# Performance work log

Measured on AMD Instinct MI355X. Metric: run time of the kernel, lower is better.

## Reference

```python
import jax, jax.numpy as jnp
import numpy as np

N = 8192
IN_F = 256
OUT_F = 128

def setup_inputs() -> dict:
    key = jax.random.key(0)
    k1, k2, k3, k4, k5 = jax.random.split(key, 5)
    adjacency_matrix = jax.random.uniform(k1, (N, N), dtype=jnp.float32)
    node_features = jax.random.normal(k2, (N, IN_F), dtype=jnp.float32)
    # nn.Linear(in_features, out_features): W is [out, in], b is [out]
    W = jax.random.normal(k3, (OUT_F, IN_F), dtype=jnp.float32) / np.sqrt(IN_F)
    b = jax.random.normal(k4, (OUT_F,), dtype=jnp.float32) * 0.01
    attn_weights = jax.random.normal(k5, (OUT_F, OUT_F), dtype=jnp.float32)
    return {"adjacency_matrix": adjacency_matrix, "node_features": node_features,
            "W": W, "b": b, "attn_weights": attn_weights}

def reference(adjacency_matrix, node_features, W, b, attn_weights):
    # h = Linear(node_features): [N, out]
    h = node_features @ W.T + b
    # bilinear scores: h @ (A @ h^T) -> [N, N]
    scores = jnp.einsum('nd,de,me->nm', h, attn_weights, h)
    attn = jax.nn.softmax(scores, axis=1)
    # weighted aggregation: [N, N] @ [N, out]
    h_agg = attn @ h
    return h_agg
```

## Files before the change

kernel.cpp:

```cpp
#include <hip/hip_runtime.h>
#include <hip/hip_bf16.h>
#include <stdint.h>


#define NN 8192
#define INF_ 256
#define D 128
#define BQ 64
#define BK 64
#define KSPLIT 4
#define KSEG (NN / KSPLIT)
#define L2E 1.44269504088896340736f

typedef __attribute__((ext_vector_type(8))) short bf16x8;
typedef __attribute__((ext_vector_type(4))) float f32x4;
typedef __attribute__((ext_vector_type(4))) unsigned int uint4v;

__global__ __launch_bounds__(256) void prep_kernel(
    const float* __restrict__ X, const float* __restrict__ W,
    const float* __restrict__ bias, const float* __restrict__ A,
    __hip_bfloat16* __restrict__ h_hi, __hip_bfloat16* __restrict__ h_lo,
    __hip_bfloat16* __restrict__ q_hi, __hip_bfloat16* __restrict__ q_lo,
    __hip_bfloat16* __restrict__ ht)
{
    __shared__ float xs[32][INF_];
    __shared__ float hs[32][D];
    const int tid  = threadIdx.x;
    const int row0 = blockIdx.x * 32;

    {
        const f32x4* Xv = (const f32x4*)(X + (size_t)row0 * INF_);
        f32x4* xsv = (f32x4*)&xs[0][0];
        #pragma unroll
        for (int i = 0; i < 8; ++i) xsv[tid + i*256] = Xv[tid + i*256];
    }
    __syncthreads();

    const int c  = tid & 127;
    const int rh = tid >> 7;

    float acc[16];
    #pragma unroll
    for (int r = 0; r < 16; ++r) acc[r] = 0.f;
    const f32x4* Wv = (const f32x4*)(W + (size_t)c * INF_);
    for (int k4 = 0; k4 < INF_/4; ++k4) {
        f32x4 w4 = Wv[k4];
        #pragma unroll
        for (int r = 0; r < 16; ++r) {
            f32x4 x4 = ((const f32x4*)&xs[rh*16 + r][0])[k4];
            acc[r] += x4[0]*w4[0] + x4[1]*w4[1] + x4[2]*w4[2] + x4[3]*w4[3];
        }
    }
    const float bc = bias[c];
    #pragma unroll
    for (int r = 0; r < 16; ++r) {
        const int row = rh*16 + r;
        const float hv = acc[r] + bc;
        hs[row][c] = hv;
        const __hip_bfloat16 hi = __float2bfloat16(hv);
        const float lo = hv - __bfloat162float(hi);
        h_hi[(size_t)(row0+row)*D + c] = hi;
        h_lo[(size_t)(row0+row)*D + c] = __float2bfloat16(lo);
        ht  [(size_t)c*NN + row0 + row] = hi;
    }
    __syncthreads();

    float acc2[16];
    #pragma unroll
    for (int r = 0; r < 16; ++r) acc2[r] = 0.f;
    for (int d4 = 0; d4 < D/4; ++d4) {
        f32x4 hv4[16];
        #pragma unroll
        for (int r = 0; r < 16; ++r) hv4[r] = ((const f32x4*)&hs[rh*16 + r][0])[d4];
        #pragma unroll
        for (int dd = 0; dd < 4; ++dd) {
            const float a = A[(size_t)(d4*4 + dd)*D + c];
            #pragma unroll
            for (int r = 0; r < 16; ++r) acc2[r] += hv4[r][dd] * a;
        }
    }
    #pragma unroll
    for (int r = 0; r < 16; ++r) {
        const int row = rh*16 + r;
        const float tv = acc2[r];
        const __hip_bfloat16 hi = __float2bfloat16(tv);
        const float lo = tv - __bfloat162float(hi);
        q_hi[(size_t)(row0+row)*D + c] = hi;
        q_lo[(size_t)(row0+row)*D + c] = __float2bfloat16(lo);
    }
}

__global__ __launch_bounds__(256) void flash_kernel(
    const __hip_bfloat16* __restrict__ q_hi, const __hip_bfloat16* __restrict__ q_lo,
    const __hip_bfloat16* __restrict__ k_hi, const __hip_bfloat16* __restrict__ k_lo,
    const __hip_bfloat16* __restrict__ ht,
    float* __restrict__ opart, float* __restrict__ mpart, float* __restrict__ lpart)
{
    __shared__ __hip_bfloat16 khi[BK][136];
    __shared__ __hip_bfloat16 klo[BK][136];
    __shared__ __hip_bfloat16 vt[D][72];
    __shared__ __hip_bfloat16 pbuf[4][16][72];

    const int tid  = threadIdx.x;
    const int wave = tid >> 6;
    const int lane = tid & 63;
    const int l16  = lane & 15;
    const int quad = lane >> 4;
    const int q0    = blockIdx.x * BQ;
    const int split = blockIdx.y;
    const int jbase = split * KSEG;

    bf16x8 aqh[4], aql[4];
    {
        const size_t qrow = (size_t)q0 + wave*16 + l16;
        const __hip_bfloat16* qhp = q_hi + qrow*D;
        const __hip_bfloat16* qlp = q_lo + qrow*D;
        #pragma unroll
        for (int t = 0; t < 4; ++t) {
            aqh[t] = *(const bf16x8*)(qhp + t*32 + quad*8);
            aql[t] = *(const bf16x8*)(qlp + t*32 + quad*8);
        }
    }

    f32x4 oacc[8];
    #pragma unroll
    for (int i = 0; i < 8; ++i) oacc[i] = (f32x4){0.f, 0.f, 0.f, 0.f};
    float mi[4], li[4];
    #pragma unroll
    for (int r = 0; r < 4; ++r) { mi[r] = -1e30f; li[r] = 0.f; }

    for (int it = 0; it < KSEG/BK; ++it) {
        const int j0 = jbase + it * BK;
        __syncthreads();
        #pragma unroll
        for (int i = 0; i < 4; ++i) {
            const int chunk = tid + i*256;
            const int r  = chunk >> 4, c8 = chunk & 15;
            *(uint4v*)(&khi[r][c8*8]) = *(const uint4v*)(k_hi + (size_t)(j0+r)*D + c8*8);
            *(uint4v*)(&klo[r][c8*8]) = *(const uint4v*)(k_lo + (size_t)(j0+r)*D + c8*8);
            const int dd = chunk >> 3, cc = chunk & 7;
            *(uint4v*)(&vt[dd][cc*8]) = *(const uint4v*)(ht + (size_t)dd*NN + j0 + cc*8);
        }
        __syncthreads();

        f32x4 s[4];
        #pragma unroll
        for (int jt = 0; jt < 4; ++jt) {
            f32x4 acc = (f32x4){0.f, 0.f, 0.f, 0.f};
            #pragma unroll
            for (int t = 0; t < 4; ++t) {
                const bf16x8 bh = *(const bf16x8*)(&khi[jt*16 + l16][t*32 + quad*8]);
                const bf16x8 bl = *(const bf16x8*)(&klo[jt*16 + l16][t*32 + quad*8]);
                acc = __builtin_amdgcn_mfma_f32_16x16x32_bf16(aql[t], bh, acc, 0, 0, 0);
                acc = __builtin_amdgcn_mfma_f32_16x16x32_bf16(aqh[t], bl, acc, 0, 0, 0);
                acc = __builtin_amdgcn_mfma_f32_16x16x32_bf16(aqh[t], bh, acc, 0, 0, 0);
            }
            s[jt] = acc;
        }

        float p[4][4];
        #pragma unroll
        for (int r = 0; r < 4; ++r) {
            float v = fmaxf(fmaxf(s[0][r], s[1][r]), fmaxf(s[2][r], s[3][r]));
            #pragma unroll
            for (int m = 1; m < 16; m <<= 1) v = fmaxf(v, __shfl_xor(v, m, 64));
            const float mnew  = fmaxf(mi[r], v);
            const float alpha = exp2f((mi[r] - mnew) * L2E);
            mi[r] = mnew;
            #pragma unroll
            for (int dt = 0; dt < 8; ++dt) oacc[dt][r] *= alpha;
            float sum = 0.f;
            #pragma unroll
            for (int jt = 0; jt < 4; ++jt) {
                const float pv = exp2f((s[jt][r] - mnew) * L2E);
                p[jt][r] = pv;
                sum += pv;
            }
            #pragma unroll
            for (int m = 1; m < 16; m <<= 1) sum += __shfl_xor(sum, m, 64);
            li[r] = li[r] * alpha + sum;
        }

        #pragma unroll
        for (int r = 0; r < 4; ++r)
            #pragma unroll
            for (int jt = 0; jt < 4; ++jt)
                pbuf[wave][quad*4 + r][jt*16 + l16] = __float2bfloat16(p[jt][r]);
        __syncthreads();

        bf16x8 ap[2];
        #pragma unroll
        for (int u = 0; u < 2; ++u)
            ap[u] = *(const bf16x8*)(&pbuf[wave][l16][u*32 + quad*8]);
        #pragma unroll
        for (int dt = 0; dt < 8; ++dt)
            #pragma unroll
            for (int u = 0; u < 2; ++u) {
                const bf16x8 bv = *(const bf16x8*)(&vt[dt*16 + l16][u*32 + quad*8]);
                oacc[dt] = __builtin_amdgcn_mfma_f32_16x16x32_bf16(ap[u], bv, oacc[dt], 0, 0, 0);
            }
    }

    const int qrow_base = q0 + wave*16;
    float* op = opart + ((size_t)split * NN + qrow_base) * D;
    #pragma unroll
    for (int r = 0; r < 4; ++r) {
        const int m = quad*4 + r;
        #pragma unroll
        for (int dt = 0; dt < 8; ++dt)
            op[(size_t)m*D + dt*16 + l16] = oacc[dt][r];
    }
    if (l16 == 0) {
        #pragma unroll
        for (int r = 0; r < 4; ++r) {
            mpart[(size_t)split*NN + qrow_base + quad*4 + r] = mi[r];
            lpart[(size_t)split*NN + qrow_base + quad*4 + r] = li[r];
        }
    }
}

__global__ __launch_bounds__(256) void combine_kernel(
    const float* __restrict__ opart, const float* __restrict__ mpart,
    const float* __restrict__ lpart, float* __restrict__ out)
{
    const int idx = blockIdx.x * 256 + threadIdx.x;
    const int q = idx >> 7;
    float m = -1e30f;
    #pragma unroll
    for (int s = 0; s < KSPLIT; ++s) m = fmaxf(m, mpart[(size_t)s*NN + q]);
    float z = 0.f, o = 0.f;
    #pragma unroll
    for (int s = 0; s < KSPLIT; ++s) {
        const float w = exp2f((mpart[(size_t)s*NN + q] - m) * L2E);
        z += lpart[(size_t)s*NN + q] * w;
        o += opart[(size_t)s*NN*D + idx] * w;
    }
    out[idx] = o / z;
}

extern "C" void kernel_launch(void* const* d_in, const int* in_sizes, int n_in,
                              void* d_out, int out_size, void* d_ws, size_t ws_size,
                              hipStream_t stream)
{
    const float* X = (const float*)d_in[1];
    const float* W = (const float*)d_in[2];
    const float* b = (const float*)d_in[3];
    const float* A = (const float*)d_in[4];
    float* out = (float*)d_out;

    char* ws = (char*)d_ws;
    __hip_bfloat16* h_hi = (__hip_bfloat16*)(ws);
    __hip_bfloat16* h_lo = (__hip_bfloat16*)(ws + (size_t)(2u  << 20));
    __hip_bfloat16* q_hi = (__hip_bfloat16*)(ws + (size_t)(4u  << 20));
    __hip_bfloat16* q_lo = (__hip_bfloat16*)(ws + (size_t)(6u  << 20));
    __hip_bfloat16* ht   = (__hip_bfloat16*)(ws + (size_t)(8u  << 20));
    float* opart = (float*)(ws + (size_t)(10u << 20));
    float* mpart = (float*)(ws + (size_t)(26u << 20));
    float* lpart = (float*)(ws + (size_t)(26u << 20) + (256u << 10));

    prep_kernel<<<NN/32, 256, 0, stream>>>(X, W, b, A, h_hi, h_lo, q_hi, q_lo, ht);
    flash_kernel<<<dim3(NN/BQ, KSPLIT), 256, 0, stream>>>(
        q_hi, q_lo, h_hi, h_lo, ht, opart, mpart, lpart);
    combine_kernel<<<(NN*D)/256, 256, 0, stream>>>(opart, mpart, lpart, out);
}
```

Before: 481.7 us.

## Compute transposed scores so softmax P stays in registers, double query rows per wave

The flash kernel now computes S^T with K as the MFMA A operand, so each lane holds a full column of probabilities. That lets P feed the PV MFMA straight from registers, removing the LDS pbuf round trip and the extra barrier. Each wave now handles 32 query rows (BQ=128), which reuses every loaded K/V fragment twice, and KSPLIT goes from 4 to 8 to keep the grid size the same. The costs are higher register pressure (launch bounds set to 2 blocks), more partial output traffic into a larger combine step, and V fragments built from two 8-byte LDS reads.

```diff
diff --git a/kernel.cpp b/kernel.cpp
--- a/kernel.cpp
+++ b/kernel.cpp
@@ -6,13 +6,14 @@
 #define NN 8192
 #define INF_ 256
 #define D 128
-#define BQ 64
+#define BQ 128
 #define BK 64
-#define KSPLIT 4
+#define KSPLIT 8
 #define KSEG (NN / KSPLIT)
 #define L2E 1.44269504088896340736f
 
 typedef __attribute__((ext_vector_type(8))) short bf16x8;
+typedef __attribute__((ext_vector_type(4))) short bf16x4;
 typedef __attribute__((ext_vector_type(4))) float f32x4;
 typedef __attribute__((ext_vector_type(4))) unsigned int uint4v;
 
@@ -90,7 +91,7 @@
     }
 }
 
-__global__ __launch_bounds__(256) void flash_kernel(
+__global__ __launch_bounds__(256, 2) void flash_kernel(
     const __hip_bfloat16* __restrict__ q_hi, const __hip_bfloat16* __restrict__ q_lo,
     const __hip_bfloat16* __restrict__ k_hi, const __hip_bfloat16* __restrict__ k_lo,
     const __hip_bfloat16* __restrict__ ht,
@@ -99,7 +100,6 @@
     __shared__ __hip_bfloat16 khi[BK][136];
     __shared__ __hip_bfloat16 klo[BK][136];
     __shared__ __hip_bfloat16 vt[D][72];
-    __shared__ __hip_bfloat16 pbuf[4][16][72];
 
     const int tid  = threadIdx.x;
     const int wave = tid >> 6;
@@ -110,27 +110,28 @@
     const int split = blockIdx.y;
     const int jbase = split * KSEG;
 
-    bf16x8 aqh[4], aql[4];
-    {
-        const size_t qrow = (size_t)q0 + wave*16 + l16;
+    bf16x8 bqh[2][4], bql[2][4];
+    #pragma unroll
+    for (int it = 0; it < 2; ++it) {
+        const size_t qrow = (size_t)q0 + wave*32 + it*16 + l16;
         const __hip_bfloat16* qhp = q_hi + qrow*D;
         const __hip_bfloat16* qlp = q_lo + qrow*D;
         #pragma unroll
         for (int t = 0; t < 4; ++t) {
-            aqh[t] = *(const bf16x8*)(qhp + t*32 + quad*8);
-            aql[t] = *(const bf16x8*)(qlp + t*32 + quad*8);
-        }
-    }
-
-    f32x4 oacc[8];
-    #pragma unroll
-    for (int i = 0; i < 8; ++i) oacc[i] = (f32x4){0.f, 0.f, 0.f, 0.f};
-    float mi[4], li[4];
-    #pragma unroll
-    for (int r = 0; r < 4; ++r) { mi[r] = -1e30f; li[r] = 0.f; }
-
-    for (int it = 0; it < KSEG/BK; ++it) {
-        const int j0 = jbase + it * BK;
+            bqh[it][t] = *(const bf16x8*)(qhp + t*32 + quad*8);
+            bql[it][t] = *(const bf16x8*)(qlp + t*32 + quad*8);
+        }
+    }
+
+    f32x4 oacc[2][8];
+    #pragma unroll
+    for (int it = 0; it < 2; ++it)
+        #pragma unroll
+        for (int i = 0; i < 8; ++i) oacc[it][i] = (f32x4){0.f, 0.f, 0.f, 0.f};
+    float mi[2] = {-1e30f, -1e30f}, li[2] = {0.f, 0.f};
+
+    for (int tile = 0; tile < KSEG/BK; ++tile) {
+        const int j0 = jbase + tile * BK;
         __syncthreads();
         #pragma unroll
         for (int i = 0; i < 4; ++i) {
@@ -143,78 +144,99 @@
         }
         __syncthreads();
 
-        f32x4 s[4];
+        f32x4 st[2][4];
         #pragma unroll
         for (int jt = 0; jt < 4; ++jt) {
-            f32x4 acc = (f32x4){0.f, 0.f, 0.f, 0.f};
             #pragma unroll
             for (int t = 0; t < 4; ++t) {
-                const bf16x8 bh = *(const bf16x8*)(&khi[jt*16 + l16][t*32 + quad*8]);
-                const bf16x8 bl = *(const bf16x8*)(&klo[jt*16 + l16][t*32 + quad*8]);
-                acc = __builtin_amdgcn_mfma_f32_16x16x32_bf16(aql[t], bh, acc, 0, 0, 0);
-                acc = __builtin_amdgcn_mfma_f32_16x16x32_bf16(aqh[t], bl, acc, 0, 0, 0);
-                acc = __builtin_amdgcn_mfma_f32_16x16x32_bf16(aqh[t], bh, acc, 0, 0, 0);
-            }
-            s[jt] = acc;
-        }
-
-        float p[4][4];
+                const bf16x8 ah = *(const bf16x8*)(&khi[jt*16 + l16][t*32 + quad*8]);
+                const bf16x8 al = *(const bf16x8*)(&klo[jt*16 + l16][t*32 + quad*8]);
+                #pragma unroll
+                for (int it = 0; it < 2; ++it) {
+                    f32x4 acc = (t == 0) ? (f32x4){0.f,0.f,0.f,0.f} : st[it][jt];
+                    acc = __builtin_amdgcn_mfma_f32_16x16x32_bf16(ah, bql[it][t], acc, 0, 0, 0);
+                    acc = __builtin_amdgcn_mfma_f32_16x16x32_bf16(al, bqh[it][t], acc, 0, 0, 0);
+                    acc = __builtin_amdgcn_mfma_f32_16x16x32_bf16(ah, bqh[it][t], acc, 0, 0, 0);
+                    st[it][jt] = acc;
+                }
+            }
+        }
+
+        bf16x8 pb[2][2];
+        #pragma unroll
+        for (int it = 0; it < 2; ++it) {
+            float vmax = st[it][0][0];
+            #pragma unroll
+            for (int jt = 0; jt < 4; ++jt)
+                #pragma unroll
+                for (int r = 0; r < 4; ++r) vmax = fmaxf(vmax, st[it][jt][r]);
+            vmax = fmaxf(vmax, __shfl_xor(vmax, 16, 64));
+            vmax = fmaxf(vmax, __shfl_xor(vmax, 32, 64));
+            const float mnew  = fmaxf(mi[it], vmax);
+            const float alpha = exp2f((mi[it] - mnew) * L2E);
+            mi[it] = mnew;
+            float sum = 0.f;
+            #pragma unroll
+            for (int jt = 0; jt < 4; ++jt)
+                #pragma unroll
+                for (int r = 0; r < 4; ++r) {
+                    const float pv = exp2f((st[it][jt][r] - mnew) * L2E);
+                    st[it][jt][r] = pv;
+                    sum += pv;
+                }
+            sum += __shfl_xor(sum, 16, 64);
+            sum += __shfl_xor(sum, 32, 64);
+            li[it] = li[it] * alpha + sum;
+
+            #pragma unroll
+            for (int r = 0; r < 4; ++r) {
+                const float ar = __shfl(alpha, quad*4 + r, 64);
+                #pragma unroll
+                for (int dt = 0; dt < 8; ++dt) oacc[it][dt][r] *= ar;
+            }
+            #pragma unroll
+            for (int jp = 0; jp < 2; ++jp) {
+                bf16x8 f;
+                #pragma unroll
+                for (int r = 0; r < 4; ++r) {
+                    f[r]     = __bfloat16_as_short(__float2bfloat16(st[it][2*jp  ][r]));
+                    f[r + 4] = __bfloat16_as_short(__float2bfloat16(st[it][2*jp+1][r]));
+                }
+                pb[it][jp] = f;
+            }
+        }
+
+        #pragma unroll
+        for (int dt = 0; dt < 8; ++dt) {
+            const __hip_bfloat16* vrow = &vt[dt*16 + l16][0];
+            #pragma unroll
+            for (int jp = 0; jp < 2; ++jp) {
+                const bf16x4 v0 = *(const bf16x4*)(vrow + (2*jp)*16   + quad*4);
+                const bf16x4 v1 = *(const bf16x4*)(vrow + (2*jp+1)*16 + quad*4);
+                bf16x8 bv;
+                #pragma unroll
+                for (int r = 0; r < 4; ++r) { bv[r] = v0[r]; bv[r+4] = v1[r]; }
+                #pragma unroll
+                for (int it = 0; it < 2; ++it)
+                    oacc[it][dt] = __builtin_amdgcn_mfma_f32_16x16x32_bf16(
+                        pb[it][jp], bv, oacc[it][dt], 0, 0, 0);
+            }
+        }
+    }
+
+    float* op = opart + ((size_t)split * NN + q0 + wave*32) * D;
+    #pragma unroll
+    for (int it = 0; it < 2; ++it) {
         #pragma unroll
         for (int r = 0; r < 4; ++r) {
-            float v = fmaxf(fmaxf(s[0][r], s[1][r]), fmaxf(s[2][r], s[3][r]));
-            #pragma unroll
-            for (int m = 1; m < 16; m <<= 1) v = fmaxf(v, __shfl_xor(v, m, 64));
-            const float mnew  = fmaxf(mi[r], v);
-            const float alpha = exp2f((mi[r] - mnew) * L2E);
-            mi[r] = mnew;
-            #pragma unroll
-            for (int dt = 0; dt < 8; ++dt) oacc[dt][r] *= alpha;
-            float sum = 0.f;
-            #pragma unroll
-            for (int jt = 0; jt < 4; ++jt) {
-                const float pv = exp2f((s[jt][r] - mnew) * L2E);
-                p[jt][r] = pv;
-                sum += pv;
-            }
-            #pragma unroll
-            for (int m = 1; m < 16; m <<= 1) sum += __shfl_xor(sum, m, 64);
-            li[r] = li[r] * alpha + sum;
-        }
-
-        #pragma unroll
-        for (int r = 0; r < 4; ++r)
-            #pragma unroll
-            for (int jt = 0; jt < 4; ++jt)
-                pbuf[wave][quad*4 + r][jt*16 + l16] = __float2bfloat16(p[jt][r]);
-        __syncthreads();
-
-        bf16x8 ap[2];
-        #pragma unroll
-        for (int u = 0; u < 2; ++u)
-            ap[u] = *(const bf16x8*)(&pbuf[wave][l16][u*32 + quad*8]);
-        #pragma unroll
-        for (int dt = 0; dt < 8; ++dt)
-            #pragma unroll
-            for (int u = 0; u < 2; ++u) {
-                const bf16x8 bv = *(const bf16x8*)(&vt[dt*16 + l16][u*32 + quad*8]);
-                oacc[dt] = __builtin_amdgcn_mfma_f32_16x16x32_bf16(ap[u], bv, oacc[dt], 0, 0, 0);
-            }
-    }
-
-    const int qrow_base = q0 + wave*16;
-    float* op = opart + ((size_t)split * NN + qrow_base) * D;
-    #pragma unroll
-    for (int r = 0; r < 4; ++r) {
-        const int m = quad*4 + r;
-        #pragma unroll
-        for (int dt = 0; dt < 8; ++dt)
-            op[(size_t)m*D + dt*16 + l16] = oacc[dt][r];
-    }
-    if (l16 == 0) {
-        #pragma unroll
-        for (int r = 0; r < 4; ++r) {
-            mpart[(size_t)split*NN + qrow_base + quad*4 + r] = mi[r];
-            lpart[(size_t)split*NN + qrow_base + quad*4 + r] = li[r];
+            const int m = it*16 + quad*4 + r;
+            #pragma unroll
+            for (int dt = 0; dt < 8; ++dt)
+                op[(size_t)m*D + dt*16 + l16] = oacc[it][dt][r];
+        }
+        if (quad == 0) {
+            mpart[(size_t)split*NN + q0 + wave*32 + it*16 + l16] = mi[it];
+            lpart[(size_t)split*NN + q0 + wave*32 + it*16 + l16] = li[it];
         }
     }
 }
@@ -255,8 +277,8 @@
     __hip_bfloat16* q_lo = (__hip_bfloat16*)(ws + (size_t)(6u  << 20));
     __hip_bfloat16* ht   = (__hip_bfloat16*)(ws + (size_t)(8u  << 20));
     float* opart = (float*)(ws + (size_t)(10u << 20));
-    float* mpart = (float*)(ws + (size_t)(26u << 20));
-    float* lpart = (float*)(ws + (size_t)(26u << 20) + (256u << 10));
+    float* mpart = (float*)(ws + (size_t)(42u << 20));
+    float* lpart = (float*)(ws + (size_t)(42u << 20) + (256u << 10));
 
     prep_kernel<<<NN/32, 256, 0, stream>>>(X, W, b, A, h_hi, h_lo, q_hi, q_lo, ht);
     flash_kernel<<<dim3(NN/BQ, KSPLIT), 256, 0, stream>>>(
```

After: 462.0 us. -4.1%, faster.
